# Kernel optimization log

Hardware: AMD Instinct MI355X
Metric: run time of the kernel (lower is better)

The kernel has to match this reference:

```python
import jax, jax.numpy as jnp
import numpy as np
from jax import lax

COMMITMENT_WEIGHT = 0.25
EMA_DECAY = 0.99
EPS = 1e-5


def setup_inputs() -> dict:
    key = jax.random.key(0)
    k1, k2, k3 = jax.random.split(key, 3)
    B, L, D, K = 32, 512, 384, 8192
    z = jax.random.normal(k1, (B, L, D), dtype=jnp.float32)
    codebook = jax.random.normal(k2, (K, D), dtype=jnp.float32)
    ema_cluster_size = jnp.zeros((K,), dtype=jnp.float32)
    ema_embed_sum = jax.random.normal(k3, (K, D), dtype=jnp.float32)
    return {"z": z, "codebook": codebook, "ema_cluster_size": ema_cluster_size, "ema_embed_sum": ema_embed_sum}


def reference(z, codebook, ema_cluster_size, ema_embed_sum):
    B, L, D = z.shape
    K = codebook.shape[0]
    flat_z = z.reshape(-1, D)  # [N, D]

    # squared L2 distance to every code: [N, K]
    dist = (
        jnp.sum(flat_z * flat_z, axis=-1, keepdims=True)
        + jnp.sum(codebook * codebook, axis=-1)[None, :]
        - 2.0 * (flat_z @ codebook.T)
    )
    indices = jnp.argmin(dist, axis=-1)  # [N]
    quantized = codebook[indices].reshape(B, L, D)

    # EMA codebook update (training-mode, no-grad in original)
    cluster_size = jax.ops.segment_sum(jnp.ones_like(indices, dtype=flat_z.dtype), indices, num_segments=K)
    embed_sum = jax.ops.segment_sum(flat_z, indices, num_segments=K)  # [K, D]
    new_cluster_size = ema_cluster_size * EMA_DECAY + (1.0 - EMA_DECAY) * cluster_size
    new_embed_sum = ema_embed_sum * EMA_DECAY + (1.0 - EMA_DECAY) * embed_sum
    n = jnp.sum(new_cluster_size)
    cluster_size_smoothed = (new_cluster_size + EPS) / (n + K * EPS) * n
    new_codebook = new_embed_sum / cluster_size_smoothed[:, None]

    commitment_loss = jnp.mean((z - lax.stop_gradient(quantized)) ** 2)
    codebook_loss = jnp.mean((quantized - lax.stop_gradient(z)) ** 2)
    loss = codebook_loss + COMMITMENT_WEIGHT * commitment_loss

    # straight-through estimator
    quantized_st = z + lax.stop_gradient(quantized - z)
    return (quantized_st, indices.reshape(B, L), loss, new_cluster_size, new_embed_sum, new_codebook)
```

## Files before the change

### kernel.cpp

```cpp
#include <hip/hip_runtime.h>
#include <math.h>

#define N_TOK 16384
#define DDIM  384
#define KCODE 8192
#define EMA   0.99f
#define EPS_F 1e-5f
#define MARGIN 0.5f
#define NB 32

typedef _Float16 f16x8 __attribute__((ext_vector_type(8)));
typedef float    f32x4 __attribute__((ext_vector_type(4)));

#define OFF_PD1    0UL
#define OFF_PI1    2097152UL
#define OFF_PD2    4194304UL
#define OFF_CBH    6291456UL
#define OFF_TOKL   0UL
#define OFF_OFFS   65536UL
#define OFF_CURS   98560UL
#define OFF_WSIDX  12582912UL
#define OFF_COUNTS 12648448UL
#define OFF_SUMSQ  12681216UL
#define OFF_NACC   12681220UL
#define OFF_CNORM  12681472UL
#define OFF_FLIST  12714240UL
#define OFF_FCNT   12779776UL
#define OFF_PSUM   12780032UL
#define OFF_FD1    12796416UL

typedef __attribute__((address_space(1))) const unsigned int gas_uint;
typedef __attribute__((address_space(3))) unsigned int       las_uint;
__device__ __forceinline__ void gload_lds16(const void* g, void* l) {
    __builtin_amdgcn_global_load_lds((gas_uint*)g, (las_uint*)l, 16, 0, 0);
}

__global__ void cnorm_kernel(const float* __restrict__ cb, float* __restrict__ cnorm) {
    int wave = (blockIdx.x * blockDim.x + threadIdx.x) >> 6;
    int lane = threadIdx.x & 63;
    if (wave >= KCODE) return;
    const float* row = cb + (size_t)wave * DDIM;
    float s = 0.f;
    #pragma unroll
    for (int r = 0; r < 6; r++) { float v = row[lane + 64 * r]; s += v * v; }
    #pragma unroll
    for (int off = 32; off > 0; off >>= 1) s += __shfl_down(s, off, 64);
    if (lane == 0) cnorm[wave] = s;
}

__global__ void convert_kernel(const float* __restrict__ z, const float* __restrict__ cb,
                               _Float16* __restrict__ zh, _Float16* __restrict__ cbh) {
    size_t e = ((size_t)blockIdx.x * blockDim.x + threadIdx.x) * 8;
    const size_t NZ = (size_t)N_TOK * DDIM;
    const float* s;
    _Float16* d;
    if (e < NZ) { s = z + e; d = zh + e; }
    else        { s = cb + (e - NZ); d = cbh + (e - NZ); }
    float4 v0 = *(const float4*)(s);
    float4 v1 = *(const float4*)(s + 4);
    f16x8 h;
    h[0]=(_Float16)v0.x; h[1]=(_Float16)v0.y; h[2]=(_Float16)v0.z; h[3]=(_Float16)v0.w;
    h[4]=(_Float16)v1.x; h[5]=(_Float16)v1.y; h[6]=(_Float16)v1.z; h[7]=(_Float16)v1.w;
    *(f16x8*)d = h;
}

__launch_bounds__(512)
__global__ void argmin16_kernel(const _Float16* __restrict__ zh, const _Float16* __restrict__ cbh,
                                const float* __restrict__ cnorm,
                                float* __restrict__ pd1, int* __restrict__ pi1,
                                float* __restrict__ pd2) {
    __shared__ _Float16 As[128 * 32];
    __shared__ _Float16 Bs[256 * 32];

    const int tid  = threadIdx.x;
    const int lane = tid & 63;
    const int wv   = tid >> 6;
    const int wy   = wv >> 2;
    const int wx   = wv & 3;
    const int m0   = blockIdx.x * 128;
    const int n0   = blockIdx.y * 256;
    const int l15  = lane & 15;
    const int l4   = lane >> 4;
    const int csw  = (l15 >> 1) & 3;

    f32x4 acc[4][4];
    #pragma unroll
    for (int i = 0; i < 4; i++)
        #pragma unroll
        for (int j = 0; j < 4; j++) acc[i][j] = (f32x4){0.f, 0.f, 0.f, 0.f};

    const int arow = tid >> 2;
    const int jch  = (tid & 3) ^ ((tid >> 3) & 3);
    const _Float16* a_src  = zh  + (size_t)(m0 + arow) * DDIM + jch * 8;
    const _Float16* b_src0 = cbh + (size_t)(n0 + arow) * DDIM + jch * 8;
    const _Float16* b_src1 = cbh + (size_t)(n0 + 128 + arow) * DDIM + jch * 8;
    const int dofs = wv * 512;

    gload_lds16(a_src,  As + dofs);
    gload_lds16(b_src0, Bs + dofs);
    gload_lds16(b_src1, Bs + dofs + 4096);

    for (int it = 0; it < 12; it++) {
        __syncthreads();
        f16x8 af[4], bf[4];
        #pragma unroll
        for (int im = 0; im < 4; im++)
            af[im] = *(const f16x8*)(As + (wy * 64 + im * 16 + l15) * 32 + (l4 ^ csw) * 8);
        #pragma unroll
        for (int in = 0; in < 4; in++)
            bf[in] = *(const f16x8*)(Bs + (wx * 64 + in * 16 + l15) * 32 + (l4 ^ csw) * 8);
        __syncthreads();
        if (it < 11) {
            int kc = (it + 1) * 32;
            gload_lds16(a_src + kc,  As + dofs);
            gload_lds16(b_src0 + kc, Bs + dofs);
            gload_lds16(b_src1 + kc, Bs + dofs + 4096);
        }
        #pragma unroll
        for (int im = 0; im < 4; im++)
            #pragma unroll
            for (int in = 0; in < 4; in++)
                acc[im][in] = __builtin_amdgcn_mfma_f32_16x16x32_f16(af[im], bf[in], acc[im][in], 0, 0, 0);
    }

    float* xd1 = (float*)&As[0];
    float* xd2 = xd1 + 512;
    int*   xi1 = (int*)(xd1 + 1024);

    float cn[4]; int cid[4];
    #pragma unroll
    for (int in = 0; in < 4; in++) {
        cid[in] = n0 + wx * 64 + in * 16 + l15;
        cn[in] = cnorm[cid[in]];
    }
    #pragma unroll
    for (int im = 0; im < 4; im++) {
        #pragma unroll
        for (int reg = 0; reg < 4; reg++) {
            float d1 = cn[0] - 2.f * acc[im][0][reg];
            int   i1 = cid[0];
            float d2 = 3.4e38f;
            #pragma unroll
            for (int in = 1; in < 4; in++) {
                float dd = cn[in] - 2.f * acc[im][in][reg];
                if (dd < d1) { d2 = d1; d1 = dd; i1 = cid[in]; }
                else d2 = fminf(d2, dd);
            }
            #pragma unroll
            for (int off = 1; off < 16; off <<= 1) {
                float od1 = __shfl_xor(d1, off, 16);
                int   oi1 = __shfl_xor(i1, off, 16);
                float od2 = __shfl_xor(d2, off, 16);
                if (od1 < d1 || (od1 == d1 && oi1 < i1)) { d2 = fminf(d1, od2); d1 = od1; i1 = oi1; }
                else d2 = fminf(d2, od1);
            }
            if (l15 == 0) {
                int tl = wy * 64 + im * 16 + l4 * 4 + reg;
                xd1[tl * 4 + wx] = d1; xi1[tl * 4 + wx] = i1; xd2[tl * 4 + wx] = d2;
            }
        }
    }
    __syncthreads();
    if (tid < 128) {
        float d1 = xd1[tid * 4], d2 = xd2[tid * 4];
        int   i1 = xi1[tid * 4];
        #pragma unroll
        for (int x = 1; x < 4; x++) {
            float od1 = xd1[tid * 4 + x], od2 = xd2[tid * 4 + x];
            int   oi1 = xi1[tid * 4 + x];
            if (od1 < d1 || (od1 == d1 && oi1 < i1)) { d2 = fminf(d1, od2); d1 = od1; i1 = oi1; }
            else d2 = fminf(d2, od1);
        }
        size_t o = (size_t)blockIdx.y * N_TOK + m0 + tid;
        pd1[o] = d1; pi1[o] = i1; pd2[o] = d2;
    }
}

__global__ void topmerge_kernel(const float* __restrict__ pd1, const int* __restrict__ pi1,
                                const float* __restrict__ pd2,
                                int* __restrict__ ws_idx, float* __restrict__ out_idx,
                                int* __restrict__ fcnt, int* __restrict__ flist,
                                float* __restrict__ fd1) {
    int t = blockIdx.x * blockDim.x + threadIdx.x;
    if (t >= N_TOK) return;
    float d1 = pd1[t], d2 = pd2[t];
    int   i1 = pi1[t];
    for (int nb = 1; nb < NB; nb++) {
        size_t o = (size_t)nb * N_TOK + t;
        float od1 = pd1[o], od2 = pd2[o];
        int   oi1 = pi1[o];
        if (od1 < d1 || (od1 == d1 && oi1 < i1)) { d2 = fminf(d1, od2); d1 = od1; i1 = oi1; }
        else d2 = fminf(d2, od1);
    }
    ws_idx[t] = i1;
    out_idx[t] = (float)i1;
    fd1[t] = d1;
    if (d2 - d1 < MARGIN) {
        int s = atomicAdd(fcnt, 1);
        flist[s] = t;
    }
}

__launch_bounds__(256)
__global__ void rescore2_kernel(const float* __restrict__ z, const float* __restrict__ cb,
                                const float* __restrict__ cnorm,
                                const float* __restrict__ pd1, const float* __restrict__ fd1,
                                const int* __restrict__ flist, const int* __restrict__ fcnt,
                                int* __restrict__ ws_idx, float* __restrict__ out_idx) {
    __shared__ float zt[4 * 384];
    const int lane = threadIdx.x & 63;
    const int wv   = threadIdx.x >> 6;
    const int count = fcnt[0];
    float* zrow = zt + wv * 384;
    for (int slot = blockIdx.x * 4 + wv; slot < count; slot += 2048 * 4) {
        int t = flist[slot];
        const float* zr = z + (size_t)t * DDIM;
        #pragma unroll
        for (int r = 0; r < 6; r++) zrow[lane + 64 * r] = zr[lane + 64 * r];
        float band = fd1[t] + MARGIN;
        float bd = 3.4e38f; int bi = 0x7fffffff;
        for (int nb = 0; nb < NB; nb++) {
            if (pd1[(size_t)nb * N_TOK + t] >= band) continue;
            #pragma unroll
            for (int c4 = 0; c4 < 4; c4++) {
                int c = nb * 256 + c4 * 64 + lane;
                const float* cr = cb + (size_t)c * DDIM;
                float a = 0.f;
                for (int d4 = 0; d4 < 96; d4++) {
                    float4 cv = *(const float4*)(cr + d4 * 4);
                    float4 zv = *(const float4*)(zrow + d4 * 4);
                    a = fmaf(zv.x, cv.x, a);
                    a = fmaf(zv.y, cv.y, a);
                    a = fmaf(zv.z, cv.z, a);
                    a = fmaf(zv.w, cv.w, a);
                }
                float dd = cnorm[c] - 2.f * a;
                if (dd < bd) { bd = dd; bi = c; }
            }
        }
        #pragma unroll
        for (int off = 32; off > 0; off >>= 1) {
            float od = __shfl_xor(bd, off, 64);
            int   oi = __shfl_xor(bi, off, 64);
            if (od < bd || (od == bd && oi < bi)) { bd = od; bi = oi; }
        }
        if (lane == 0) { ws_idx[t] = bi; out_idx[t] = (float)bi; }
    }
}

__global__ void quantize_kernel(const float* __restrict__ z, const float* __restrict__ cb,
                                const int* __restrict__ ws_idx,
                                float* __restrict__ out_q,
                                float* __restrict__ counts, float* __restrict__ psum) {
    __shared__ float sm[4];
    int t = (blockIdx.x * blockDim.x + threadIdx.x) >> 6;
    int lane = threadIdx.x & 63, wv = threadIdx.x >> 6;
    int k = ws_idx[t];
    const float* zr = z + (size_t)t * DDIM;
    const float* cr = cb + (size_t)k * DDIM;
    float* qr = out_q + (size_t)t * DDIM;
    float s = 0.f;
    #pragma unroll
    for (int r = 0; r < 6; r++) {
        int d = lane + 64 * r;
        float zv = zr[d];
        float qv = cr[d];
        qr[d] = qv;
        float df = zv - qv;
        s += df * df;
    }
    #pragma unroll
    for (int off = 32; off > 0; off >>= 1) s += __shfl_down(s, off, 64);
    if (lane == 0) {
        sm[wv] = s;
        atomicAdd(counts + k, 1.0f);
    }
    __syncthreads();
    if (threadIdx.x == 0) psum[blockIdx.x] = sm[0] + sm[1] + sm[2] + sm[3];
}

__global__ void scan_kernel(const float* __restrict__ counts,
                            int* __restrict__ offs, int* __restrict__ curs) {
    __shared__ int ps[1024];
    const int t = threadIdx.x;
    const int base = t * 8;
    int loc[8]; int s = 0;
    #pragma unroll
    for (int i = 0; i < 8; i++) { int c = (int)(counts[base + i] + 0.5f); loc[i] = s; s += c; }
    ps[t] = s;
    __syncthreads();
    for (int off = 1; off < 1024; off <<= 1) {
        int v = ps[t];
        int add = (t >= off) ? ps[t - off] : 0;
        __syncthreads();
        ps[t] = v + add;
        __syncthreads();
    }
    int excl = (t == 0) ? 0 : ps[t - 1];
    #pragma unroll
    for (int i = 0; i < 8; i++) {
        int o = excl + loc[i];
        offs[base + i] = o;
        curs[base + i] = o;
    }
    if (t == 1023) offs[KCODE] = ps[1023];
}

__global__ void fill_kernel(const int* __restrict__ ws_idx,
                            int* __restrict__ curs, int* __restrict__ toklist) {
    int t = blockIdx.x * blockDim.x + threadIdx.x;
    if (t >= N_TOK) return;
    int k = ws_idx[t];
    int slot = atomicAdd(curs + k, 1);
    toklist[slot] = t;
}

__global__ void cluster_kernel(const float* __restrict__ ema_cs, const float* __restrict__ counts,
                               float* __restrict__ out_ncs, float* __restrict__ n_acc,
                               const float* __restrict__ psum, float* __restrict__ out_loss) {
    int i = blockIdx.x * blockDim.x + threadIdx.x;
    float v = 0.f;
    if (i < KCODE) {
        v = EMA * ema_cs[i] + (1.f - EMA) * counts[i];
        out_ncs[i] = v;
    }
    __shared__ float sm[4];
    __shared__ float sm2[4];
    int lane = threadIdx.x & 63, w = threadIdx.x >> 6;
    #pragma unroll
    for (int off = 32; off > 0; off >>= 1) v += __shfl_down(v, off, 64);
    if (lane == 0) sm[w] = v;
    __syncthreads();
    if (threadIdx.x == 0) atomicAdd(n_acc, sm[0] + sm[1] + sm[2] + sm[3]);
    if (blockIdx.x == 0) {
        float s = 0.f;
        for (int j = threadIdx.x; j < 4096; j += 256) s += psum[j];
        #pragma unroll
        for (int off = 32; off > 0; off >>= 1) s += __shfl_down(s, off, 64);
        if (lane == 0) sm2[w] = s;
        __syncthreads();
        if (threadIdx.x == 0)
            out_loss[0] = 1.25f * (sm2[0] + sm2[1] + sm2[2] + sm2[3]) / (float)(N_TOK * DDIM);
    }
}

__global__ void codebook_fused_kernel(const float* __restrict__ z,
                                      const int* __restrict__ offs, const int* __restrict__ toklist,
                                      const float* __restrict__ ema_es,
                                      const float* __restrict__ ncs, const float* __restrict__ n_acc,
                                      float* __restrict__ out_es, float* __restrict__ out_cb) {
    int k = (blockIdx.x * blockDim.x + threadIdx.x) >> 6;
    int lane = threadIdx.x & 63;
    if (k >= KCODE) return;
    int o0 = offs[k], o1 = offs[k + 1];
    float sum[6] = {0.f, 0.f, 0.f, 0.f, 0.f, 0.f};
    for (int s = o0; s < o1; s++) {
        int tok = toklist[s];
        const float* zr = z + (size_t)tok * DDIM;
        #pragma unroll
        for (int r = 0; r < 6; r++) sum[r] += zr[lane + 64 * r];
    }
    float n = n_acc[0];
    float smooth = (ncs[k] + EPS_F) / (n + (float)KCODE * EPS_F) * n;
    float inv = 1.f / smooth;
    const float* er = ema_es + (size_t)k * DDIM;
    float* oes = out_es + (size_t)k * DDIM;
    float* ocb = out_cb + (size_t)k * DDIM;
    #pragma unroll
    for (int r = 0; r < 6; r++) {
        int d = lane + 64 * r;
        float es = EMA * er[d] + (1.f - EMA) * sum[r];
        oes[d] = es;
        ocb[d] = es * inv;
    }
}

extern "C" void kernel_launch(void* const* d_in, const int* in_sizes, int n_in,
                              void* d_out, int out_size, void* d_ws, size_t ws_size,
                              hipStream_t stream) {
    const float* z       = (const float*)d_in[0];
    const float* cb      = (const float*)d_in[1];
    const float* ema_cs  = (const float*)d_in[2];
    const float* ema_es  = (const float*)d_in[3];

    float* out      = (float*)d_out;
    float* out_q    = out;
    float* out_idx  = out + 6291456;
    float* out_loss = out + 6307840;
    float* out_ncs  = out + 6307841;
    float* out_es   = out + 6316033;
    float* out_cb   = out + 9461761;

    char* w = (char*)d_ws;
    float* pd1    = (float*)(w + OFF_PD1);
    int*   pi1    = (int*)  (w + OFF_PI1);
    float* pd2    = (float*)(w + OFF_PD2);
    _Float16* cbh = (_Float16*)(w + OFF_CBH);
    int*   toklist= (int*)  (w + OFF_TOKL);
    int*   offs   = (int*)  (w + OFF_OFFS);
    int*   curs   = (int*)  (w + OFF_CURS);
    float* cnorm  = (float*)(w + OFF_CNORM);
    int*   flist  = (int*)  (w + OFF_FLIST);
    int*   fcnt   = (int*)  (w + OFF_FCNT);
    int*   ws_idx = (int*)  (w + OFF_WSIDX);
    float* counts = (float*)(w + OFF_COUNTS);
    float* psum   = (float*)(w + OFF_PSUM);
    float* n_acc  = (float*)(w + OFF_NACC);
    float* fd1    = (float*)(w + OFF_FD1);

    _Float16* zh = (_Float16*)out;

    hipMemsetAsync(w + OFF_FCNT, 0, 256, stream);
    hipMemsetAsync(w + OFF_COUNTS, 0, 32768 + 256, stream);

    cnorm_kernel<<<KCODE * 64 / 256, 256, 0, stream>>>(cb, cnorm);

    convert_kernel<<<4608, 256, 0, stream>>>(z, cb, zh, cbh);

    dim3 grid_am(N_TOK / 128, KCODE / 256, 1);
    argmin16_kernel<<<grid_am, 512, 0, stream>>>(zh, cbh, cnorm, pd1, pi1, pd2);

    topmerge_kernel<<<N_TOK / 256, 256, 0, stream>>>(pd1, pi1, pd2, ws_idx, out_idx, fcnt, flist, fd1);

    rescore2_kernel<<<2048, 256, 0, stream>>>(z, cb, cnorm, pd1, fd1, flist, fcnt, ws_idx, out_idx);

    quantize_kernel<<<N_TOK * 64 / 256, 256, 0, stream>>>(z, cb, ws_idx, out_q, counts, psum);
    scan_kernel<<<1, 1024, 0, stream>>>(counts, offs, curs);
    fill_kernel<<<N_TOK / 256, 256, 0, stream>>>(ws_idx, curs, toklist);
    cluster_kernel<<<(KCODE + 255) / 256, 256, 0, stream>>>(ema_cs, counts, out_ncs, n_acc, psum, out_loss);
    codebook_fused_kernel<<<KCODE * 64 / 256, 256, 0, stream>>>(z, offs, toklist, ema_es, out_ncs, n_acc, out_es, out_cb);
}
```

Baseline: 587.3 us.

## Fuse codebook norm into fp16 convert and double K-step in argmin GEMM

Merges the codebook-norm kernel and the fp32-to-fp16 convert kernel into one row-per-wave kernel, so the codebook is read once and one launch is saved. The argmin GEMM now stages 64-wide K slices instead of 32, halving the number of barrier-separated iterations, with a new XOR swizzle for the wider LDS rows and a launch_bounds occupancy hint. The larger LDS footprint (48KB per block) and the extra live fragments may reduce occupancy. The fused convert writes scalar fp16 values rather than vectors, which may lower store efficiency.

```diff
diff --git a/kernel.cpp b/kernel.cpp
--- a/kernel.cpp
+++ b/kernel.cpp
@@ -35,42 +35,39 @@
     __builtin_amdgcn_global_load_lds((gas_uint*)g, (las_uint*)l, 16, 0, 0);
 }
 
-__global__ void cnorm_kernel(const float* __restrict__ cb, float* __restrict__ cnorm) {
-    int wave = (blockIdx.x * blockDim.x + threadIdx.x) >> 6;
+__global__ void convert_norm_kernel(const float* __restrict__ z, const float* __restrict__ cb,
+                                    _Float16* __restrict__ zh, _Float16* __restrict__ cbh,
+                                    float* __restrict__ cnorm) {
+    int row  = (blockIdx.x * blockDim.x + threadIdx.x) >> 6;
     int lane = threadIdx.x & 63;
-    if (wave >= KCODE) return;
-    const float* row = cb + (size_t)wave * DDIM;
+    const float* src;
+    _Float16* dst;
+    bool is_cb = (row >= N_TOK);
+    if (is_cb) { int k = row - N_TOK; src = cb + (size_t)k * DDIM; dst = cbh + (size_t)k * DDIM; }
+    else       {                      src = z  + (size_t)row * DDIM; dst = zh + (size_t)row * DDIM; }
     float s = 0.f;
     #pragma unroll
-    for (int r = 0; r < 6; r++) { float v = row[lane + 64 * r]; s += v * v; }
-    #pragma unroll
-    for (int off = 32; off > 0; off >>= 1) s += __shfl_down(s, off, 64);
-    if (lane == 0) cnorm[wave] = s;
-}
-
-__global__ void convert_kernel(const float* __restrict__ z, const float* __restrict__ cb,
-                               _Float16* __restrict__ zh, _Float16* __restrict__ cbh) {
-    size_t e = ((size_t)blockIdx.x * blockDim.x + threadIdx.x) * 8;
-    const size_t NZ = (size_t)N_TOK * DDIM;
-    const float* s;
-    _Float16* d;
-    if (e < NZ) { s = z + e; d = zh + e; }
-    else        { s = cb + (e - NZ); d = cbh + (e - NZ); }
-    float4 v0 = *(const float4*)(s);
-    float4 v1 = *(const float4*)(s + 4);
-    f16x8 h;
-    h[0]=(_Float16)v0.x; h[1]=(_Float16)v0.y; h[2]=(_Float16)v0.z; h[3]=(_Float16)v0.w;
-    h[4]=(_Float16)v1.x; h[5]=(_Float16)v1.y; h[6]=(_Float16)v1.z; h[7]=(_Float16)v1.w;
-    *(f16x8*)d = h;
-}
-
-__launch_bounds__(512)
+    for (int r = 0; r < 3; r++) {
+        int e = (lane + 64 * r) * 2;
+        float2 v = *(const float2*)(src + e);
+        s = fmaf(v.x, v.x, fmaf(v.y, v.y, s));
+        _Float16 h0 = (_Float16)v.x, h1 = (_Float16)v.y;
+        dst[e] = h0; dst[e + 1] = h1;
+    }
+    if (is_cb) {
+        #pragma unroll
+        for (int off = 32; off > 0; off >>= 1) s += __shfl_down(s, off, 64);
+        if (lane == 0) cnorm[row - N_TOK] = s;
+    }
+}
+
+__launch_bounds__(512, 4)
 __global__ void argmin16_kernel(const _Float16* __restrict__ zh, const _Float16* __restrict__ cbh,
                                 const float* __restrict__ cnorm,
                                 float* __restrict__ pd1, int* __restrict__ pi1,
                                 float* __restrict__ pd2) {
-    __shared__ _Float16 As[128 * 32];
-    __shared__ _Float16 Bs[256 * 32];
+    __shared__ _Float16 As[128 * 64];
+    __shared__ _Float16 Bs[256 * 64];
 
     const int tid  = threadIdx.x;
     const int lane = tid & 63;
@@ -81,7 +78,7 @@
     const int n0   = blockIdx.y * 256;
     const int l15  = lane & 15;
     const int l4   = lane >> 4;
-    const int csw  = (l15 >> 1) & 3;
+    const int rsw  = l15 & 7;
 
     f32x4 acc[4][4];
     #pragma unroll
@@ -89,32 +86,49 @@
         #pragma unroll
         for (int j = 0; j < 4; j++) acc[i][j] = (f32x4){0.f, 0.f, 0.f, 0.f};
 
-    const int arow = tid >> 2;
-    const int jch  = (tid & 3) ^ ((tid >> 3) & 3);
-    const _Float16* a_src  = zh  + (size_t)(m0 + arow) * DDIM + jch * 8;
-    const _Float16* b_src0 = cbh + (size_t)(n0 + arow) * DDIM + jch * 8;
-    const _Float16* b_src1 = cbh + (size_t)(n0 + 128 + arow) * DDIM + jch * 8;
-    const int dofs = wv * 512;
-
-    gload_lds16(a_src,  As + dofs);
-    gload_lds16(b_src0, Bs + dofs);
-    gload_lds16(b_src1, Bs + dofs + 4096);
-
-    for (int it = 0; it < 12; it++) {
+    const int r8  = lane >> 3;
+    const int jch = (lane & 7) ^ (r8 & 7);
+    const _Float16* a_g = zh  + (size_t)(m0 + wv * 8 + r8) * DDIM + jch * 8;
+    const _Float16* b_g = cbh + (size_t)(n0 + wv * 8 + r8) * DDIM + jch * 8;
+    _Float16* a_d = As + wv * 512;
+    _Float16* b_d = Bs + wv * 512;
+
+    gload_lds16(a_g,                      a_d);
+    gload_lds16(a_g + (size_t)64 * DDIM,  a_d + 4096);
+    gload_lds16(b_g,                      b_d);
+    gload_lds16(b_g + (size_t)64 * DDIM,  b_d + 4096);
+    gload_lds16(b_g + (size_t)128 * DDIM, b_d + 8192);
+    gload_lds16(b_g + (size_t)192 * DDIM, b_d + 12288);
+
+    for (int it = 0; it < 6; it++) {
         __syncthreads();
         f16x8 af[4], bf[4];
         #pragma unroll
         for (int im = 0; im < 4; im++)
-            af[im] = *(const f16x8*)(As + (wy * 64 + im * 16 + l15) * 32 + (l4 ^ csw) * 8);
+            af[im] = *(const f16x8*)(As + (wy * 64 + im * 16 + l15) * 64 + (l4 ^ rsw) * 8);
         #pragma unroll
         for (int in = 0; in < 4; in++)
-            bf[in] = *(const f16x8*)(Bs + (wx * 64 + in * 16 + l15) * 32 + (l4 ^ csw) * 8);
+            bf[in] = *(const f16x8*)(Bs + (wx * 64 + in * 16 + l15) * 64 + (l4 ^ rsw) * 8);
+        #pragma unroll
+        for (int im = 0; im < 4; im++)
+            #pragma unroll
+            for (int in = 0; in < 4; in++)
+                acc[im][in] = __builtin_amdgcn_mfma_f32_16x16x32_f16(af[im], bf[in], acc[im][in], 0, 0, 0);
+        #pragma unroll
+        for (int im = 0; im < 4; im++)
+            af[im] = *(const f16x8*)(As + (wy * 64 + im * 16 + l15) * 64 + ((4 + l4) ^ rsw) * 8);
+        #pragma unroll
+        for (int in = 0; in < 4; in++)
+            bf[in] = *(const f16x8*)(Bs + (wx * 64 + in * 16 + l15) * 64 + ((4 + l4) ^ rsw) * 8);
         __syncthreads();
-        if (it < 11) {
-            int kc = (it + 1) * 32;
-            gload_lds16(a_src + kc,  As + dofs);
-            gload_lds16(b_src0 + kc, Bs + dofs);
-            gload_lds16(b_src1 + kc, Bs + dofs + 4096);
+        if (it < 5) {
+            int kc = (it + 1) * 64;
+            gload_lds16(a_g + kc,                      a_d);
+            gload_lds16(a_g + (size_t)64 * DDIM + kc,  a_d + 4096);
+            gload_lds16(b_g + kc,                      b_d);
+            gload_lds16(b_g + (size_t)64 * DDIM + kc,  b_d + 4096);
+            gload_lds16(b_g + (size_t)128 * DDIM + kc, b_d + 8192);
+            gload_lds16(b_g + (size_t)192 * DDIM + kc, b_d + 12288);
         }
         #pragma unroll
         for (int im = 0; im < 4; im++)
@@ -413,9 +427,7 @@
     hipMemsetAsync(w + OFF_FCNT, 0, 256, stream);
     hipMemsetAsync(w + OFF_COUNTS, 0, 32768 + 256, stream);
 
-    cnorm_kernel<<<KCODE * 64 / 256, 256, 0, stream>>>(cb, cnorm);
-
-    convert_kernel<<<4608, 256, 0, stream>>>(z, cb, zh, cbh);
+    convert_norm_kernel<<<(N_TOK + KCODE) / 4, 256, 0, stream>>>(z, cb, zh, cbh, cnorm);
 
     dim3 grid_am(N_TOK / 128, KCODE / 256, 1);
     argmin16_kernel<<<grid_am, 512, 0, stream>>>(zh, cbh, cnorm, pd1, pi1, pd2);
```

After: 572.0 us. 1.03x faster.
